# Optimization experiments

Hardware: AMD Instinct MI355X
Metric: run time of the kernel (lower is better)

## Reference

```python
import jax, jax.numpy as jnp
import numpy as np

EMBED_DIM = 512
N_QUERY = 4096
N_PROTO = 1024


def setup_inputs() -> dict:
    key = jax.random.key(0)
    k_q, k_p, k_wmu = jax.random.split(key, 3)
    d = EMBED_DIM
    bound = (6.0 / (d + d)) ** 0.5
    return {
        "query_features": jax.random.normal(k_q, (N_QUERY, d), dtype=jnp.float32),
        "prototypes": jax.random.normal(k_p, (N_PROTO, d), dtype=jnp.float32),
        "weight_mu": jax.random.uniform(k_wmu, (d, d), dtype=jnp.float32, minval=-bound, maxval=bound),
        "weight_rho": jnp.full((d, d), -3.0, dtype=jnp.float32),
        "bias_mu": jnp.zeros((d,), dtype=jnp.float32),
        "bias_rho": jnp.full((d,), 0.01, dtype=jnp.float32),
        "n_samples": 10,
    }


def reference(query_features, prototypes, weight_mu, weight_rho, bias_mu, bias_rho, n_samples):
    d = weight_mu.shape[0]
    # softplus reparameterization (same each iteration in the original loop)
    weight_sigma = jnp.log1p(jnp.exp(weight_rho))  # [d, d]
    bias_sigma = jnp.log1p(jnp.exp(bias_rho))      # [d]
    # batched MC weight/bias samples: [S, d, d] and [S, d]
    key = jax.random.key(42)
    kw, kb = jax.random.split(key)
    eps_w = jax.random.normal(kw, (n_samples, d, d), dtype=weight_mu.dtype)
    eps_b = jax.random.normal(kb, (n_samples, d), dtype=bias_mu.dtype)
    w = weight_mu[None] + weight_sigma[None] * eps_w   # [S, d, d]
    b = bias_mu[None] + bias_sigma[None] * eps_b       # [S, d]
    # F.linear(x, W_sample.T, b) == x @ W_sample + b
    tq = jnp.einsum('qd,sde->sqe', query_features, w) + b[:, None, :]  # [S, Q, d]
    # cdist via ||a||^2 + ||b||^2 - 2 a.b
    sq_q = jnp.sum(tq * tq, axis=-1)                    # [S, Q]
    sq_p = jnp.sum(prototypes * prototypes, axis=-1)    # [P]
    cross = jnp.einsum('sqe,pe->sqp', tq, prototypes)   # [S, Q, P]
    sqd = sq_q[:, :, None] + sq_p[None, None, :] - 2.0 * cross
    dists = jnp.sqrt(jnp.maximum(sqd, 1e-12))           # [S, Q, P]
    mean_distance = jnp.mean(dists, axis=0)
    uncertainty = jnp.std(dists, axis=0, ddof=1)        # torch.std is unbiased
    return mean_distance, uncertainty
```

## Files before the change

### kernel.cpp

```cpp
#include <hip/hip_runtime.h>
#include <stdint.h>

#define NS 10
#define DIM 512
#define NQ 4096
#define NP 1024

typedef unsigned short ushort_t;
typedef __bf16 bf16el_t;
typedef bf16el_t bf16x8 __attribute__((ext_vector_type(8)));
typedef float floatx4 __attribute__((ext_vector_type(4)));

__host__ __device__ __forceinline__ uint32_t rotl32(uint32_t x, int r) {
  return (x << r) | (x >> (32 - r));
}

__host__ __device__ __forceinline__ void threefry2x32(uint32_t k0, uint32_t k1,
                                                      uint32_t x0, uint32_t x1,
                                                      uint32_t* o0, uint32_t* o1) {
  uint32_t ks2 = k0 ^ k1 ^ 0x1BD11BDAu;
  x0 += k0; x1 += k1;
#define TF_R(r) { x0 += x1; x1 = rotl32(x1, r); x1 ^= x0; }
  TF_R(13) TF_R(15) TF_R(26) TF_R(6)   x0 += k1;  x1 += ks2 + 1u;
  TF_R(17) TF_R(29) TF_R(16) TF_R(24)  x0 += ks2; x1 += k0 + 2u;
  TF_R(13) TF_R(15) TF_R(26) TF_R(6)   x0 += k0;  x1 += k1 + 3u;
  TF_R(17) TF_R(29) TF_R(16) TF_R(24)  x0 += k1;  x1 += ks2 + 4u;
  TF_R(13) TF_R(15) TF_R(26) TF_R(6)   x0 += ks2; x1 += k0 + 5u;
#undef TF_R
  *o0 = x0; *o1 = x1;
}

__device__ __forceinline__ uint32_t jax_random_bits(uint32_t k0, uint32_t k1, uint32_t idx) {
  uint32_t o0, o1;
  threefry2x32(k0, k1, 0u, idx, &o0, &o1);
  return o0 ^ o1;
}

__device__ __forceinline__ float erfinvf_xla(float x) {
  float w = -log1pf(-x * x);
  float p;
  if (w < 5.0f) {
    w -= 2.5f;
    p = 2.81022636e-08f;
    p = fmaf(p, w, 3.43273939e-07f);
    p = fmaf(p, w, -3.5233877e-06f);
    p = fmaf(p, w, -4.39150654e-06f);
    p = fmaf(p, w, 0.00021858087f);
    p = fmaf(p, w, -0.00125372503f);
    p = fmaf(p, w, -0.00417768164f);
    p = fmaf(p, w, 0.246640727f);
    p = fmaf(p, w, 1.50140941f);
  } else {
    w = sqrtf(w) - 3.0f;
    p = -0.000200214257f;
    p = fmaf(p, w, 0.000100950558f);
    p = fmaf(p, w, 0.00134934322f);
    p = fmaf(p, w, -0.00367342844f);
    p = fmaf(p, w, 0.00573950773f);
    p = fmaf(p, w, -0.0076224613f);
    p = fmaf(p, w, 0.00943887047f);
    p = fmaf(p, w, 1.00167406f);
    p = fmaf(p, w, 2.83297682f);
  }
  return p * x;
}

__device__ __forceinline__ float jax_bits_to_normal(uint32_t bits) {
  float f = __uint_as_float((bits >> 9) | 0x3F800000u) - 1.0f;
  float u = f * 2.0f - 0.99999994f;
  u = fmaxf(u, -0.99999994f);
  return 1.41421356f * erfinvf_xla(u);
}

__device__ __forceinline__ float softplusf(float x) { return log1pf(expf(x)); }

__device__ __forceinline__ float bf2f(ushort_t u) {
  return __uint_as_float(((uint32_t)u) << 16);
}
__device__ __forceinline__ ushort_t f2bf(float f) {
  uint32_t u = __float_as_uint(f);
  u += 0x7FFFu + ((u >> 16) & 1u);
  return (ushort_t)(u >> 16);
}

__device__ __forceinline__ void gll16(const void* g, void* l) {
  __builtin_amdgcn_global_load_lds(
      (const __attribute__((address_space(1))) uint32_t*)g,
      (__attribute__((address_space(3))) uint32_t*)l, 16, 0, 0);
}

__global__ __launch_bounds__(256) void prep_kernel(const float* __restrict__ qf,
                                                   const float* __restrict__ pf,
                                                   const float* __restrict__ wmu,
                                                   const float* __restrict__ wrho,
                                                   const float* __restrict__ bmu,
                                                   const float* __restrict__ brho,
                                                   ushort_t* __restrict__ wt,
                                                   ushort_t* __restrict__ qb,
                                                   ushort_t* __restrict__ pb,
                                                   float* __restrict__ sqp,
                                                   float* __restrict__ bvec,
                                                   float* __restrict__ sqq,
                                                   uint32_t kw0, uint32_t kw1,
                                                   uint32_t kb0, uint32_t kb1) {
  const int blk = blockIdx.x;
  const int tid = threadIdx.x;
  if (blk < 10240) {
    uint32_t t = blk * 256u + tid;
    uint32_t s = t >> 18;
    uint32_t r = t & 0x3FFFFu;
    uint32_t e = r >> 9;
    uint32_t k = r & 511u;
    uint32_t eps_idx = (s << 18) | (k << 9) | e;
    uint32_t bits = jax_random_bits(kw0, kw1, eps_idx);
    float n = jax_bits_to_normal(bits);
    uint32_t mi = (k << 9) | e;
    float w = wmu[mi] + softplusf(wrho[mi]) * n;
    wt[t] = f2bf(w);
  } else if (blk < 12288) {
    int i = ((blk - 10240) * 256 + tid) * 4;
    float4 v = *(const float4*)&qf[i];
    uint2 r;
    r.x = (uint32_t)f2bf(v.x) | ((uint32_t)f2bf(v.y) << 16);
    r.y = (uint32_t)f2bf(v.z) | ((uint32_t)f2bf(v.w) << 16);
    *(uint2*)&qb[i] = r;
  } else if (blk < 12544) {
    int p = (blk - 12288) * 4 + (tid >> 6);
    int lane = tid & 63;
    const float* src = pf + p * DIM + lane * 8;
    float4 a = *(const float4*)src;
    float4 b = *(const float4*)(src + 4);
    float vals[8] = {a.x, a.y, a.z, a.w, b.x, b.y, b.z, b.w};
    ushort_t o[8];
    float ss = 0.f;
#pragma unroll
    for (int i = 0; i < 8; ++i) {
      o[i] = f2bf(vals[i]);
      float f = bf2f(o[i]);
      ss += f * f;
    }
    *(uint4*)&pb[p * DIM + lane * 8] = *(const uint4*)o;
#pragma unroll
    for (int off = 32; off; off >>= 1) ss += __shfl_xor(ss, off, 64);
    if (lane == 0) sqp[p] = ss;
  } else if (blk < 12564) {
    uint32_t t2 = (blk - 12544) * 256u + tid;
    uint32_t e = t2 & 511u;
    uint32_t bits = jax_random_bits(kb0, kb1, t2);
    float n = jax_bits_to_normal(bits);
    bvec[t2] = bmu[e] + softplusf(brho[e]) * n;
  } else {
    int i = (blk - 12564) * 256 + tid;
    sqq[i] = 0.f;
  }
}

__global__ __launch_bounds__(256) void gemm_tq_kernel(const ushort_t* __restrict__ qb,
                                                      const ushort_t* __restrict__ wt,
                                                      const float* __restrict__ bvec,
                                                      ushort_t* __restrict__ tq,
                                                      float* __restrict__ sqq) {
  __shared__ __align__(16) ushort_t ls[2 * 128 * 64];
  ushort_t* lsA = ls;
  ushort_t* lsB = ls + 128 * 64;
  const int lane = threadIdx.x & 63;
  const int wave = threadIdx.x >> 6;
  const int wm = wave >> 1, wn = wave & 1;
  const int qBase = blockIdx.x * 128;
  const int eBase = blockIdx.y * 128;
  const int s = blockIdx.z;
  const ushort_t* wbase = wt + (size_t)s * (DIM * DIM);
  const int srow = lane >> 3;
  const int scol = ((lane & 7) ^ srow) * 16;
  const char* gA = (const char*)qb + (size_t)(qBase + wave * 32 + srow) * (DIM * 2) + scol;
  const char* gB = (const char*)wbase + (size_t)(eBase + wave * 32 + srow) * (DIM * 2) + scol;
  char* lA = (char*)&lsA[wave * 32 * 64];
  char* lB = (char*)&lsB[wave * 32 * 64];
  const int cn = lane & 15;
  const int cn7 = cn & 7;
  const int jc = lane >> 4;
  const floatx4 fzero = {0.f, 0.f, 0.f, 0.f};
  floatx4 acc[4][4];
#pragma unroll
  for (int mi = 0; mi < 4; ++mi)
#pragma unroll
    for (int ni = 0; ni < 4; ++ni) acc[mi][ni] = fzero;

  for (int kt = 0; kt < 8; ++kt) {
    __syncthreads();
#pragma unroll
    for (int j = 0; j < 4; ++j) {
      gll16(gA + (size_t)j * 8 * (DIM * 2), lA + j * 1024);
      gll16(gB + (size_t)j * 8 * (DIM * 2), lB + j * 1024);
    }
    gA += 128; gB += 128;
    __syncthreads();
#pragma unroll
    for (int c = 0; c < 8; c += 4) {
      const int po = ((c + jc) ^ cn7) << 3;
      bf16x8 aF[4], bF[4];
#pragma unroll
      for (int mi = 0; mi < 4; ++mi)
        aF[mi] = *(const bf16x8*)&lsA[(wm * 64 + mi * 16 + cn) * 64 + po];
#pragma unroll
      for (int ni = 0; ni < 4; ++ni)
        bF[ni] = *(const bf16x8*)&lsB[(wn * 64 + ni * 16 + cn) * 64 + po];
#pragma unroll
      for (int mi = 0; mi < 4; ++mi)
#pragma unroll
        for (int ni = 0; ni < 4; ++ni)
          acc[mi][ni] = __builtin_amdgcn_mfma_f32_16x16x32_bf16(aF[mi], bF[ni], acc[mi][ni], 0, 0, 0);
    }
  }

  __syncthreads();
  ushort_t* area = ls + wave * 4096;
  float bv[4];
#pragma unroll
  for (int ni = 0; ni < 4; ++ni) bv[ni] = bvec[s * DIM + eBase + wn * 64 + ni * 16 + cn];
  const int jc4 = jc * 4;
#pragma unroll
  for (int mi = 0; mi < 4; ++mi)
#pragma unroll
    for (int ni = 0; ni < 4; ++ni)
#pragma unroll
      for (int r = 0; r < 4; ++r) {
        const int lr = mi * 16 + jc4 + r;
        const int lc = ni * 16 + cn;
        const int off = lr * 64 + (((lc >> 3) ^ (lr & 7)) << 3) + (lc & 7);
        area[off] = f2bf(acc[mi][ni][r] + bv[ni]);
      }
  __syncthreads();
  const int rr = lane >> 3;
  const int ch = lane & 7;
  const int physc = ch ^ rr;
  const size_t tqs = (size_t)s * (NQ * DIM);
#pragma unroll
  for (int pass = 0; pass < 8; ++pass) {
    const int lr = pass * 8 + rr;
    uint4 v = *(const uint4*)&area[lr * 64 + physc * 8];
    uint32_t wsv[4] = {v.x, v.y, v.z, v.w};
    float ss = 0.f;
#pragma unroll
    for (int i = 0; i < 4; ++i) {
      float lo = bf2f((ushort_t)(wsv[i] & 0xFFFFu));
      float hi = bf2f((ushort_t)(wsv[i] >> 16));
      ss += lo * lo + hi * hi;
    }
    ss += __shfl_xor(ss, 1, 64);
    ss += __shfl_xor(ss, 2, 64);
    ss += __shfl_xor(ss, 4, 64);
    const int q = qBase + wm * 64 + lr;
    *(uint4*)&tq[tqs + (size_t)q * DIM + eBase + wn * 64 + ch * 8] = v;
    if (ch == 0) atomicAdd(&sqq[s * NQ + q], ss);
  }
}

__global__ __launch_bounds__(256) void gemm_dist_kernel(const ushort_t* __restrict__ tq,
                                                        const ushort_t* __restrict__ pb,
                                                        const float* __restrict__ sqq,
                                                        const float* __restrict__ sqp,
                                                        float* __restrict__ out) {
  __shared__ __align__(16) ushort_t lsA[2 * 64 * 128];
  __shared__ __align__(16) ushort_t lsB[128 * 128];
  const int lane = threadIdx.x & 63;
  const int wave = threadIdx.x >> 6;
  const int wm = wave >> 1;
  const int wn = wave & 1;
  const int qBase = blockIdx.x * 64;
  const int pBase = blockIdx.y * 128;
  const int srow = lane >> 4;
  const int scc = lane & 15;
  const int sccx = scc ^ srow;
  const char* gAb = (const char*)tq + (size_t)(qBase + wave * 16 + srow) * (DIM * 2);
  const char* gBb = (const char*)pb + (size_t)(pBase + wave * 32 + srow) * (DIM * 2);
  char* lA = (char*)lsA + wave * 4096;
  char* lB = (char*)lsB + wave * 8192;
  const int cn = lane & 15;
  const int jc = lane >> 4;
  const int rq = jc * 4;
  const floatx4 fzero = {0.f, 0.f, 0.f, 0.f};

  float sum[2][4][4] = {};
  float ssq[2][4][4] = {};
  float sqp_v[4];
#pragma unroll
  for (int ni = 0; ni < 4; ++ni) sqp_v[ni] = sqp[pBase + wn * 64 + ni * 16 + cn];

  for (int s0 = 0; s0 < NS; s0 += 2) {
    floatx4 acc[2][2][4];
#pragma unroll
    for (int sp = 0; sp < 2; ++sp)
#pragma unroll
      for (int mi = 0; mi < 2; ++mi)
#pragma unroll
        for (int ni = 0; ni < 4; ++ni) acc[sp][mi][ni] = fzero;

    const char* gA0 = gAb + (size_t)s0 * (NQ * DIM * 2);
    const char* gA1 = gA0 + (size_t)(NQ * DIM * 2);
    const char* gBk = gBb;
    for (int kt = 0; kt < 4; ++kt) {
      __syncthreads();
#pragma unroll
      for (int g = 0; g < 4; ++g) {
        const size_t off = (size_t)g * 4 * (DIM * 2) + (size_t)((sccx ^ (g * 4)) << 4);
        gll16(gA0 + off, lA + g * 1024);
        gll16(gA1 + off, lA + 16384 + g * 1024);
      }
#pragma unroll
      for (int g = 0; g < 8; ++g)
        gll16(gBk + (size_t)g * 4 * (DIM * 2) + (size_t)((sccx ^ ((g & 3) * 4)) << 4),
              lB + g * 1024);
      gA0 += 256; gA1 += 256; gBk += 256;
      __syncthreads();
#pragma unroll
      for (int c4 = 0; c4 < 4; ++c4) {
        const int po = (((c4 * 4 + jc) ^ cn) & 15) << 3;
        bf16x8 bF[4];
#pragma unroll
        for (int ni = 0; ni < 4; ++ni)
          bF[ni] = *(const bf16x8*)&lsB[(wn * 64 + ni * 16 + cn) * 128 + po];
#pragma unroll
        for (int sp = 0; sp < 2; ++sp) {
          bf16x8 aF[2];
#pragma unroll
          for (int mi = 0; mi < 2; ++mi)
            aF[mi] = *(const bf16x8*)&lsA[sp * 8192 + (wm * 32 + mi * 16 + cn) * 128 + po];
#pragma unroll
          for (int mi = 0; mi < 2; ++mi)
#pragma unroll
            for (int ni = 0; ni < 4; ++ni)
              acc[sp][mi][ni] =
                  __builtin_amdgcn_mfma_f32_16x16x32_bf16(aF[mi], bF[ni], acc[sp][mi][ni], 0, 0, 0);
        }
      }
    }
#pragma unroll
    for (int sp = 0; sp < 2; ++sp) {
      const int s = s0 + sp;
#pragma unroll
      for (int mi = 0; mi < 2; ++mi) {
        float4 aqv = *(const float4*)&sqq[s * NQ + qBase + wm * 32 + mi * 16 + rq];
        float aqa[4] = {aqv.x, aqv.y, aqv.z, aqv.w};
#pragma unroll
        for (int r = 0; r < 4; ++r) {
          float aq = aqa[r];
#pragma unroll
          for (int ni = 0; ni < 4; ++ni) {
            float sqd = fmaxf(fmaf(-2.0f, acc[sp][mi][ni][r], aq + sqp_v[ni]), 1e-12f);
            sum[mi][ni][r] += sqrtf(sqd);
            ssq[mi][ni][r] += sqd;
          }
        }
      }
    }
  }
#pragma unroll
  for (int mi = 0; mi < 2; ++mi)
#pragma unroll
    for (int ni = 0; ni < 4; ++ni)
#pragma unroll
      for (int r = 0; r < 4; ++r) {
        int q = qBase + wm * 32 + mi * 16 + rq + r;
        int p = pBase + wn * 64 + ni * 16 + cn;
        float sm = sum[mi][ni][r];
        float mean = sm * 0.1f;
        float var = (ssq[mi][ni][r] - sm * sm * 0.1f) * (1.0f / 9.0f);
        out[(size_t)q * NP + p] = mean;
        out[(size_t)NQ * NP + (size_t)q * NP + p] = sqrtf(fmaxf(var, 0.0f));
      }
}

extern "C" void kernel_launch(void* const* d_in, const int* in_sizes, int n_in,
                              void* d_out, int out_size, void* d_ws, size_t ws_size,
                              hipStream_t stream) {
  const float* qf   = (const float*)d_in[0];
  const float* pf   = (const float*)d_in[1];
  const float* wmu  = (const float*)d_in[2];
  const float* wrho = (const float*)d_in[3];
  const float* bmu  = (const float*)d_in[4];
  const float* brho = (const float*)d_in[5];
  float* out = (float*)d_out;
  char* ws = (char*)d_ws;
  ushort_t* wt   = (ushort_t*)(ws);
  ushort_t* qb   = (ushort_t*)(ws + 5242880);
  ushort_t* pb   = (ushort_t*)(ws + 9437184);
  float*    bvec = (float*)   (ws + 10485760);
  float*    sqp  = (float*)   (ws + 10506240);
  ushort_t* tq   = (ushort_t*)(ws + 10510336);
  float*    sqq  = (float*)   (ws + 52453376);

  uint32_t kw0, kw1, kb0, kb1;
  threefry2x32(0u, 42u, 0u, 0u, &kw0, &kw1);
  threefry2x32(0u, 42u, 0u, 1u, &kb0, &kb1);

  hipLaunchKernelGGL(prep_kernel, dim3(12724), dim3(256), 0, stream,
                     qf, pf, wmu, wrho, bmu, brho, wt, qb, pb, sqp, bvec, sqq,
                     kw0, kw1, kb0, kb1);
  hipLaunchKernelGGL(gemm_tq_kernel, dim3(32, 4, 10), dim3(256), 0, stream, qb, wt, bvec, tq, sqq);
  hipLaunchKernelGGL(gemm_dist_kernel, dim3(64, 8), dim3(256), 0, stream, tq, pb, sqq, sqp, out);
}
```

Baseline: 245.2 us.

## Shrink distance-GEMM tiles to 64x64 with two waves and smaller K step

The distance GEMM kernel moves from 256-thread blocks with 64x128 output tiles and a 128-wide K step to 128-thread blocks with 64x64 tiles and a 64-wide K step. The LDS layout and swizzle are redone to match, and the grid doubles to 64x16 blocks. The aim is to launch more, smaller blocks (1024 instead of 512) so more CUs stay busy and LDS use per block drops. The cost is lower reuse of the prototype tile, more global loads per output, and twice as many barrier-separated K iterations.

```diff
diff --git a/kernel.cpp b/kernel.cpp
--- a/kernel.cpp
+++ b/kernel.cpp
@@ -256,36 +256,38 @@
   }
 }
 
-__global__ __launch_bounds__(256) void gemm_dist_kernel(const ushort_t* __restrict__ tq,
-                                                        const ushort_t* __restrict__ pb,
-                                                        const float* __restrict__ sqq,
-                                                        const float* __restrict__ sqp,
-                                                        float* __restrict__ out) {
-  __shared__ __align__(16) ushort_t lsA[2 * 64 * 128];
-  __shared__ __align__(16) ushort_t lsB[128 * 128];
+__global__ __launch_bounds__(128, 2) void gemm_dist_kernel(const ushort_t* __restrict__ tq,
+                                                           const ushort_t* __restrict__ pb,
+                                                           const float* __restrict__ sqq,
+                                                           const float* __restrict__ sqp,
+                                                           float* __restrict__ out) {
+  __shared__ __align__(16) ushort_t lsA[2 * 64 * 64];
+  __shared__ __align__(16) ushort_t lsB[64 * 64];
   const int lane = threadIdx.x & 63;
   const int wave = threadIdx.x >> 6;
-  const int wm = wave >> 1;
-  const int wn = wave & 1;
   const int qBase = blockIdx.x * 64;
-  const int pBase = blockIdx.y * 128;
-  const int srow = lane >> 4;
-  const int scc = lane & 15;
-  const int sccx = scc ^ srow;
-  const char* gAb = (const char*)tq + (size_t)(qBase + wave * 16 + srow) * (DIM * 2);
-  const char* gBb = (const char*)pb + (size_t)(pBase + wave * 32 + srow) * (DIM * 2);
-  char* lA = (char*)lsA + wave * 4096;
-  char* lB = (char*)lsB + wave * 8192;
+  const int pBase = blockIdx.y * 64;
+  const int srow = lane >> 3;
+  const int scol = ((lane & 7) ^ srow) * 16;
   const int cn = lane & 15;
+  const int cn7 = cn & 7;
   const int jc = lane >> 4;
   const int rq = jc * 4;
   const floatx4 fzero = {0.f, 0.f, 0.f, 0.f};
+  const char* gAb = (const char*)tq + (size_t)(qBase + wave * 32 + srow) * (DIM * 2) + scol;
+  const char* gBb = (const char*)pb + (size_t)(pBase + wave * 32 + srow) * (DIM * 2) + scol;
+  char* lA0 = (char*)lsA + (wave * 32) * 128;
+  char* lA1 = lA0 + 8192;
+  char* lBw = (char*)lsB + (wave * 32) * 128;
+  int po[2];
+#pragma unroll
+  for (int c = 0; c < 2; ++c) po[c] = ((c * 4 + jc) ^ cn7) << 3;
 
   float sum[2][4][4] = {};
   float ssq[2][4][4] = {};
   float sqp_v[4];
 #pragma unroll
-  for (int ni = 0; ni < 4; ++ni) sqp_v[ni] = sqp[pBase + wn * 64 + ni * 16 + cn];
+  for (int ni = 0; ni < 4; ++ni) sqp_v[ni] = sqp[pBase + ni * 16 + cn];
 
   for (int s0 = 0; s0 < NS; s0 += 2) {
     floatx4 acc[2][2][4];
@@ -299,33 +301,29 @@
     const char* gA0 = gAb + (size_t)s0 * (NQ * DIM * 2);
     const char* gA1 = gA0 + (size_t)(NQ * DIM * 2);
     const char* gBk = gBb;
-    for (int kt = 0; kt < 4; ++kt) {
+    for (int kt = 0; kt < 8; ++kt) {
       __syncthreads();
 #pragma unroll
       for (int g = 0; g < 4; ++g) {
-        const size_t off = (size_t)g * 4 * (DIM * 2) + (size_t)((sccx ^ (g * 4)) << 4);
-        gll16(gA0 + off, lA + g * 1024);
-        gll16(gA1 + off, lA + 16384 + g * 1024);
+        const size_t gRow = (size_t)g * 8 * (DIM * 2);
+        gll16(gA0 + gRow, lA0 + g * 1024);
+        gll16(gA1 + gRow, lA1 + g * 1024);
+        gll16(gBk + gRow, lBw + g * 1024);
       }
-#pragma unroll
-      for (int g = 0; g < 8; ++g)
-        gll16(gBk + (size_t)g * 4 * (DIM * 2) + (size_t)((sccx ^ ((g & 3) * 4)) << 4),
-              lB + g * 1024);
-      gA0 += 256; gA1 += 256; gBk += 256;
+      gA0 += 128; gA1 += 128; gBk += 128;
       __syncthreads();
 #pragma unroll
-      for (int c4 = 0; c4 < 4; ++c4) {
-        const int po = (((c4 * 4 + jc) ^ cn) & 15) << 3;
+      for (int c = 0; c < 2; ++c) {
         bf16x8 bF[4];
 #pragma unroll
         for (int ni = 0; ni < 4; ++ni)
-          bF[ni] = *(const bf16x8*)&lsB[(wn * 64 + ni * 16 + cn) * 128 + po];
+          bF[ni] = *(const bf16x8*)&lsB[(ni * 16 + cn) * 64 + po[c]];
 #pragma unroll
         for (int sp = 0; sp < 2; ++sp) {
           bf16x8 aF[2];
 #pragma unroll
           for (int mi = 0; mi < 2; ++mi)
-            aF[mi] = *(const bf16x8*)&lsA[sp * 8192 + (wm * 32 + mi * 16 + cn) * 128 + po];
+            aF[mi] = *(const bf16x8*)&lsA[sp * 4096 + (wave * 32 + mi * 16 + cn) * 64 + po[c]];
 #pragma unroll
           for (int mi = 0; mi < 2; ++mi)
 #pragma unroll
@@ -340,7 +338,7 @@
       const int s = s0 + sp;
 #pragma unroll
       for (int mi = 0; mi < 2; ++mi) {
-        float4 aqv = *(const float4*)&sqq[s * NQ + qBase + wm * 32 + mi * 16 + rq];
+        float4 aqv = *(const float4*)&sqq[s * NQ + qBase + wave * 32 + mi * 16 + rq];
         float aqa[4] = {aqv.x, aqv.y, aqv.z, aqv.w};
 #pragma unroll
         for (int r = 0; r < 4; ++r) {
@@ -361,8 +359,8 @@
     for (int ni = 0; ni < 4; ++ni)
 #pragma unroll
       for (int r = 0; r < 4; ++r) {
-        int q = qBase + wm * 32 + mi * 16 + rq + r;
-        int p = pBase + wn * 64 + ni * 16 + cn;
+        int q = qBase + wave * 32 + mi * 16 + rq + r;
+        int p = pBase + ni * 16 + cn;
         float sm = sum[mi][ni][r];
         float mean = sm * 0.1f;
         float var = (ssq[mi][ni][r] - sm * sm * 0.1f) * (1.0f / 9.0f);
@@ -398,5 +396,5 @@
                      qf, pf, wmu, wrho, bmu, brho, wt, qb, pb, sqp, bvec, sqq,
                      kw0, kw1, kb0, kb1);
   hipLaunchKernelGGL(gemm_tq_kernel, dim3(32, 4, 10), dim3(256), 0, stream, qb, wt, bvec, tq, sqq);
-  hipLaunchKernelGGL(gemm_dist_kernel, dim3(64, 8), dim3(256), 0, stream, tq, pb, sqq, sqp, out);
-}
+  hipLaunchKernelGGL(gemm_dist_kernel, dim3(64, 16), dim3(128), 0, stream, tq, pb, sqq, sqp, out);
+}
```

After: 202.0 us. -17.6%, faster.
